# Kernel optimization log

Measured on AMD Instinct MI355X. Metric: run time of the kernel, lower is better.

## Reference

```python
import jax, jax.numpy as jnp
import numpy as np

B, L, T, D, H, DH = 8, 1024, 1024, 768, 12, 64
SPATIAL_DIM = 5


def setup_inputs() -> dict:
    key = jax.random.key(0)
    ks = jax.random.split(key, 12)
    scale = 1.0 / np.sqrt(D)
    inp = {
        "q": jax.random.normal(ks[0], (B, L, D), dtype=jnp.float32),
        "k": jax.random.normal(ks[1], (B, T, D), dtype=jnp.float32),
        "v": jax.random.normal(ks[2], (B, T, D), dtype=jnp.float32),
        "pairwise_locs": jax.random.normal(ks[3], (B, L, T, SPATIAL_DIM), dtype=jnp.float32),
        # last 64 key positions are padding in every batch row (never all-True)
        "key_padding_mask": jnp.broadcast_to(jnp.arange(T) >= T - 64, (B, T)),
        "Wq": jax.random.normal(ks[4], (D, H * DH), dtype=jnp.float32) * scale,
        "bq": jnp.zeros((H * DH,), dtype=jnp.float32),
        "Wk": jax.random.normal(ks[5], (D, H * DH), dtype=jnp.float32) * scale,
        "bk": jnp.zeros((H * DH,), dtype=jnp.float32),
        "Wv": jax.random.normal(ks[6], (D, H * DH), dtype=jnp.float32) * scale,
        "bv": jnp.zeros((H * DH,), dtype=jnp.float32),
        "Wo": jax.random.normal(ks[7], (H * DH, D), dtype=jnp.float32) * scale,
        "bo": jnp.zeros((D,), dtype=jnp.float32),
    }
    return inp


def reference(q, k, v, pairwise_locs, key_padding_mask, Wq, bq, Wk, bk, Wv, bv, Wo, bo):
    # pairwise_locs is accepted but unused in this forward path (as in the source).
    b, l, _ = q.shape
    t = k.shape[1]
    qh = (q @ Wq + bq).reshape(b, l, H, DH)  # b l h d
    kh = (k @ Wk + bk).reshape(b, t, H, DH)  # b t h d
    vh = (v @ Wv + bv).reshape(b, t, H, DH)  # b t h d
    attn = jnp.einsum('blhd,bthd->bhlt', qh, kh) / jnp.sqrt(jnp.float32(DH))
    attn = jnp.where(key_padding_mask[:, None, None, :], -jnp.inf, attn)
    fused_attn = jax.nn.softmax(attn, axis=-1)
    out = jnp.einsum('bhlt,bthd->blhd', fused_attn, vh).reshape(b, l, H * DH)
    return out @ Wo + bo  # dropout is identity in eval mode
```

## Files before the change

kernel.cpp:

```cpp
#include <hip/hip_runtime.h>
#include <hip/hip_bf16.h>
#include <cstdint>
#include <cstddef>
#include <cmath>

#define NB 8
#define NL 1024
#define NT 1024
#define ND 768
#define NH 12
#define NDH 64
#define NM (NB*NL)

typedef short short8 __attribute__((ext_vector_type(8)));
typedef unsigned short ushort4v __attribute__((ext_vector_type(4)));
typedef unsigned int uint4v __attribute__((ext_vector_type(4)));
typedef float f32x4 __attribute__((ext_vector_type(4)));
typedef float f32x16 __attribute__((ext_vector_type(16)));
typedef float float4v __attribute__((ext_vector_type(4)));

__device__ __forceinline__ unsigned short f2bf(float f) {
  union { __hip_bfloat16 h; unsigned short u; } cv;
  cv.h = __float2bfloat16(f);
  return cv.u;
}
__device__ __forceinline__ unsigned pk2(float lo, float hi) {
  return (unsigned)f2bf(lo) | ((unsigned)f2bf(hi) << 16);
}
__device__ __forceinline__ void gll16(const void* g, void* l) {
  __builtin_amdgcn_global_load_lds(
      (const __attribute__((address_space(1))) unsigned int*)g,
      (__attribute__((address_space(3))) unsigned int*)l, 16, 0, 0);
}

__global__ __launch_bounds__(128) void maskbits_kernel(
    const unsigned int* __restrict__ mask, unsigned long long* __restrict__ mb) {
  const int id = threadIdx.x;
  const unsigned int* src = mask + (size_t)(id >> 4) * NT + (id & 15) * 64;
  unsigned long long m = 0;
  for (int j = 0; j < 64; j++) m |= (unsigned long long)(src[j] != 0u) << j;
  mb[id] = m;
}

__global__ __launch_bounds__(256) void wt_kernel(
    const float* __restrict__ W0, const float* __restrict__ W1,
    const float* __restrict__ W2, const float* __restrict__ W3,
    unsigned short* __restrict__ Wt) {
  __shared__ float tile[32][33];
  const float* W = blockIdx.z == 0 ? W0 : blockIdx.z == 1 ? W1 : blockIdx.z == 2 ? W2 : W3;
  const int k0 = blockIdx.x * 32, n0 = blockIdx.y * 32;
  const int tx = threadIdx.x & 31, ty = threadIdx.x >> 5;
  for (int r = ty; r < 32; r += 8) tile[r][tx] = W[(size_t)(k0 + r) * ND + n0 + tx];
  __syncthreads();
  unsigned short* out = Wt + (size_t)blockIdx.z * ND * ND;
  for (int r = ty; r < 32; r += 8) out[(size_t)(n0 + r) * ND + k0 + tx] = f2bf(tile[tx][r]);
}

template<int MODE>
__global__ __launch_bounds__(256) void gemm_kernel(
    const float* __restrict__ Af0, const float* __restrict__ Af1,
    const float* __restrict__ Af2, const unsigned short* __restrict__ Ab,
    const unsigned short* __restrict__ Wt,
    const float* __restrict__ bias0, const float* __restrict__ bias1,
    const float* __restrict__ bias2,
    unsigned short* __restrict__ outb0, unsigned short* __restrict__ outb1,
    unsigned short* __restrict__ outb2, float* __restrict__ outf) {
  __shared__ __align__(16) unsigned short As[128 * 64];
  __shared__ __align__(16) unsigned short Bs[128 * 64];
  const int tid = threadIdx.x, lane = tid & 63, w = tid >> 6;
  const int c = lane & 15, g = lane >> 4;
  const int wrow = w & 1, wcol = w >> 1;
  const int l8 = lane >> 3, l7 = lane & 7, csw = l7 ^ l8;
  const int mbase = blockIdx.x * 128, nbase = blockIdx.y * 128;
  const int z = (MODE == 0) ? blockIdx.z : 3;

  const float* Af = (MODE == 0) ? (z == 0 ? Af0 : z == 1 ? Af1 : Af2) : nullptr;
  const unsigned short* Bt = Wt + (size_t)z * ND * ND;
  const float* bias = (MODE == 0) ? (z == 0 ? bias0 : z == 1 ? bias1 : bias2) : bias0;

  f32x4 acc[4][4];
#pragma unroll
  for (int m = 0; m < 4; m++)
#pragma unroll
    for (int n = 0; n < 4; n++) acc[m][n] = (f32x4){0.f, 0.f, 0.f, 0.f};

  for (int k0 = 0; k0 < ND; k0 += 64) {
    if (MODE == 0) {
#pragma unroll
      for (int i = 0; i < 4; i++) {
        int id = i * 256 + tid;
        int r = id >> 3, cc = id & 7;
        const float* src = &Af[(size_t)(mbase + r) * ND + k0 + cc * 8];
        float4v x0 = *(const float4v*)src;
        float4v x1 = *(const float4v*)(src + 4);
        uint4v y = {pk2(x0[0], x0[1]), pk2(x0[2], x0[3]),
                    pk2(x1[0], x1[1]), pk2(x1[2], x1[3])};
        *(uint4v*)&As[r * 64 + ((cc ^ (r & 7)) * 8)] = y;
      }
    } else {
#pragma unroll
      for (int it = 0; it < 4; it++) {
        int r = it * 32 + w * 8 + l8;
        gll16(&Ab[(size_t)(mbase + r) * ND + k0 + csw * 8], &As[(it * 32 + w * 8) * 64]);
      }
    }
#pragma unroll
    for (int it = 0; it < 4; it++) {
      int r = it * 32 + w * 8 + l8;
      gll16(&Bt[(size_t)(nbase + r) * ND + k0 + csw * 8], &Bs[(it * 32 + w * 8) * 64]);
    }
    __syncthreads();

#pragma unroll
    for (int ks = 0; ks < 2; ks++) {
      short8 a[4], b[4];
#pragma unroll
      for (int m = 0; m < 4; m++) {
        int r = wrow * 64 + m * 16 + c;
        a[m] = *(const short8*)&As[r * 64 + (((ks * 4 + g) ^ (c & 7)) * 8)];
      }
#pragma unroll
      for (int n = 0; n < 4; n++) {
        int r = wcol * 64 + n * 16 + c;
        b[n] = *(const short8*)&Bs[r * 64 + (((ks * 4 + g) ^ (c & 7)) * 8)];
      }
      if (MODE == 0 && z == 2) {
#pragma unroll
        for (int m = 0; m < 4; m++)
#pragma unroll
          for (int n = 0; n < 4; n++)
            acc[m][n] = __builtin_amdgcn_mfma_f32_16x16x32_bf16(a[m], b[n], acc[m][n], 0, 0, 0);
      } else {
#pragma unroll
        for (int m = 0; m < 4; m++)
#pragma unroll
          for (int n = 0; n < 4; n++)
            acc[m][n] = __builtin_amdgcn_mfma_f32_16x16x32_bf16(b[n], a[m], acc[m][n], 0, 0, 0);
      }
    }
    __syncthreads();
  }

  if (MODE == 0 && z == 2) {
#pragma unroll
    for (int n = 0; n < 4; n++) {
      const int col = nbase + wcol * 64 + n * 16 + c;
      const float bv = bias[col];
      const int h = col >> 6, dd = col & 63;
#pragma unroll
      for (int m = 0; m < 4; m++) {
        const int r0 = mbase + wrow * 64 + m * 16 + g * 4;
        const int bb = r0 >> 10, t = r0 & (NT - 1);
        ushort4v y;
#pragma unroll
        for (int j = 0; j < 4; j++) y[j] = f2bf(acc[m][n][j] + bv);
        *(ushort4v*)&outb2[((size_t)(bb * NH + h) * NDH + dd) * NT + t] = y;
      }
    }
  } else {
    const float scale = (MODE == 0 && z == 0) ? 0.125f * 1.44269504f : 1.0f;
    unsigned short* outb = (MODE == 0) ? (z == 0 ? outb0 : outb1) : nullptr;
#pragma unroll
    for (int n = 0; n < 4; n++) {
      const int colb = nbase + wcol * 64 + n * 16 + g * 4;
      float4v bv4 = *(const float4v*)&bias[colb];
#pragma unroll
      for (int m = 0; m < 4; m++) {
        const int row = mbase + wrow * 64 + m * 16 + c;
        if (MODE == 3) {
          float4v y;
#pragma unroll
          for (int j = 0; j < 4; j++) y[j] = acc[m][n][j] + bv4[j];
          *(float4v*)&outf[(size_t)row * ND + colb] = y;
        } else {
          ushort4v y;
#pragma unroll
          for (int j = 0; j < 4; j++) y[j] = f2bf((acc[m][n][j] + bv4[j]) * scale);
          *(ushort4v*)&outb[(size_t)row * ND + colb] = y;
        }
      }
    }
  }
}

__global__ __launch_bounds__(256) void attn_kernel(
    const unsigned short* __restrict__ qh, const unsigned short* __restrict__ kh,
    const unsigned short* __restrict__ vhT, const unsigned long long* __restrict__ maskbits,
    unsigned short* __restrict__ ao) {
  __shared__ __align__(16) unsigned short Ks[3][64 * 64];
  __shared__ __align__(16) unsigned short Vs[3][64 * 64];
  const int tid = threadIdx.x, lane = tid & 63, w = tid >> 6;
  const int q32 = lane & 31, hi = lane >> 5;
  const int l8 = lane >> 3, l7 = lane & 7;

  const int lin = blockIdx.x;
  const int qb = ((lin >> 3) & 7) * 128;
  const int bh = (lin & 7) + 8 * (lin >> 6);
  const int b = bh / NH, h = bh % NH;
  const size_t kbase = (size_t)b * NT * ND + h * NDH;
  const size_t vbase = (size_t)(b * NH + h) * NDH * NT;

  const unsigned mwsrc = ((const unsigned*)maskbits)[(size_t)b * 32 + (lane & 31)];

  short8 aq[4];
  {
    size_t qrow = (size_t)(b * NL + qb + w * 32 + q32) * ND + h * NDH + hi * 8;
#pragma unroll
    for (int ks = 0; ks < 4; ks++)
      aq[ks] = *(const short8*)&qh[qrow + ks * 16];
  }

  f32x16 o[2] = {{}, {}};
  f32x4 lrv = {0.f, 0.f, 0.f, 0.f};
  float mr = -1e30f;

  const int srow = w * 16 + l8;
  const int scs0 = l7 ^ (srow & 7), scs1 = l7 ^ ((srow + 8) & 7);

#define STAGE(gidx, nb)                                                        \
  do {                                                                         \
    gll16(&kh[kbase + (size_t)((gidx) * 64 + srow) * ND + scs0 * 8],           \
          &Ks[nb][(w * 16) * 64]);                                             \
    gll16(&vhT[vbase + (size_t)srow * NT + (gidx) * 64 + scs0 * 8],            \
          &Vs[nb][(w * 16) * 64]);                                             \
    gll16(&kh[kbase + (size_t)((gidx) * 64 + srow + 8) * ND + scs1 * 8],       \
          &Ks[nb][(w * 16 + 8) * 64]);                                         \
    gll16(&vhT[vbase + (size_t)(srow + 8) * NT + (gidx) * 64 + scs1 * 8],      \
          &Vs[nb][(w * 16 + 8) * 64]);                                         \
  } while (0)

  STAGE(0, 0);
  STAGE(1, 1);
  asm volatile("s_waitcnt vmcnt(4)" ::: "memory");
  __builtin_amdgcn_sched_barrier(0);
  __builtin_amdgcn_s_barrier();
  __builtin_amdgcn_sched_barrier(0);

  int cur = 0;
  unsigned mlo = __shfl(mwsrc, 0, 64);
  unsigned mhi_ = __shfl(mwsrc, 1, 64);

  for (int tIdx = 0; tIdx < NT / 64; tIdx++) {
    bool issued = false;
    if (tIdx + 2 < NT / 64) {
      unsigned plo = __shfl(mwsrc, tIdx * 2 + 4, 64);
      unsigned phi = __shfl(mwsrc, tIdx * 2 + 5, 64);
      if ((plo & phi) != 0xffffffffu) {
        int nb = cur + 2; if (nb >= 3) nb -= 3;
        STAGE(tIdx + 2, nb);
        issued = true;
      }
    }
    unsigned nlo = 0xffffffffu, nhi = 0xffffffffu;
    if (tIdx + 1 < NT / 64) {
      nlo = __shfl(mwsrc, tIdx * 2 + 2, 64);
      nhi = __shfl(mwsrc, tIdx * 2 + 3, 64);
    }

    if ((mlo & mhi_) != 0xffffffffu) {
      const bool anymask = (mlo | mhi_) != 0u;
#pragma unroll
      for (int tt = 0; tt < 2; tt++) {
        f32x16 s = {};
        __builtin_amdgcn_s_setprio(1);
#pragma unroll
        for (int ks = 0; ks < 4; ks++) {
          short8 ak = *(const short8*)&Ks[cur][(tt * 32 + q32) * 64 +
                          ((((ks << 1) | hi) ^ (q32 & 7)) * 8)];
          s = __builtin_amdgcn_mfma_f32_32x32x16_bf16(ak, aq[ks], s, 0, 0, 0);
        }
        __builtin_amdgcn_s_setprio(0);

        if (anymask) {
          unsigned wsd = tt ? mhi_ : mlo;
          wsd = hi ? (wsd >> 4) : wsd;
#pragma unroll
          for (int a = 0; a < 4; a++)
#pragma unroll
            for (int j = 0; j < 4; j++)
              if ((wsd >> (8 * a + j)) & 1) s[4 * a + j] = -INFINITY;
        }

        float mt = s[0];
#pragma unroll
        for (int r = 1; r < 16; r++) mt = fmaxf(mt, s[r]);
        mt = fmaxf(mt, __shfl_xor(mt, 32, 64));
        if (!__all(mt <= mr + 8.f)) {
          float mnew = fmaxf(mr, mt);
          float alpha = exp2f(mr - mnew);
          mr = mnew;
          lrv *= alpha; o[0] *= alpha; o[1] *= alpha;
        }
        unsigned pkv[4][2];
#pragma unroll
        for (int a = 0; a < 4; a++) {
          f32x4 p;
#pragma unroll
          for (int j = 0; j < 4; j++) p[j] = exp2f(s[4 * a + j] - mr);
          lrv += p;
          pkv[a][0] = pk2(p[0], p[1]);
          pkv[a][1] = pk2(p[2], p[3]);
        }

#pragma unroll
        for (int ts = 0; ts < 2; ts++) {
          unsigned u0 = pkv[2 * ts][0], u1 = pkv[2 * ts][1];
          unsigned w0 = pkv[2 * ts + 1][0], w1 = pkv[2 * ts + 1][1];
          unsigned r0 = __shfl_xor(hi ? u0 : w0, 32, 64);
          unsigned r1 = __shfl_xor(hi ? u1 : w1, 32, 64);
          union { unsigned u[4]; short8 s8; } bp;
          bp.u[0] = hi ? r0 : u0;
          bp.u[1] = hi ? r1 : u1;
          bp.u[2] = hi ? w0 : r0;
          bp.u[3] = hi ? w1 : r1;
          __builtin_amdgcn_s_setprio(1);
#pragma unroll
          for (int dt = 0; dt < 2; dt++) {
            short8 av = *(const short8*)&Vs[cur][(dt * 32 + q32) * 64 +
                            ((((tt << 2) | (ts << 1) | hi) ^ (q32 & 7)) * 8)];
            o[dt] = __builtin_amdgcn_mfma_f32_32x32x16_bf16(av, bp.s8, o[dt], 0, 0, 0);
          }
          __builtin_amdgcn_s_setprio(0);
        }
      }
    }

    if (issued)
      asm volatile("s_waitcnt vmcnt(4) lgkmcnt(0)" ::: "memory");
    else
      asm volatile("s_waitcnt vmcnt(0) lgkmcnt(0)" ::: "memory");
    __builtin_amdgcn_sched_barrier(0);
    __builtin_amdgcn_s_barrier();
    __builtin_amdgcn_sched_barrier(0);

    mlo = nlo; mhi_ = nhi;
    cur = (cur == 2) ? 0 : cur + 1;
  }
#undef STAGE

  float lr = (lrv[0] + lrv[1]) + (lrv[2] + lrv[3]);
  lr += __shfl_xor(lr, 32, 64);
  float inv = 1.f / lr;
  size_t row = (size_t)(b * NL + qb + w * 32 + q32) * ND + h * NDH;
#pragma unroll
  for (int dt = 0; dt < 2; dt++)
#pragma unroll
    for (int a = 0; a < 4; a++) {
      ushort4v y;
#pragma unroll
      for (int j = 0; j < 4; j++) y[j] = f2bf(o[dt][4 * a + j] * inv);
      *(ushort4v*)&ao[row + dt * 32 + 8 * a + 4 * hi] = y;
    }
}

extern "C" void kernel_launch(void* const* d_in, const int* in_sizes, int n_in,
                              void* d_out, int out_size, void* d_ws, size_t ws_size,
                              hipStream_t stream) {
  const float* q  = (const float*)d_in[0];
  const float* k  = (const float*)d_in[1];
  const float* v  = (const float*)d_in[2];
  const unsigned int* mask = (const unsigned int*)d_in[4];
  const float* Wq = (const float*)d_in[5];
  const float* bq = (const float*)d_in[6];
  const float* Wk = (const float*)d_in[7];
  const float* bk = (const float*)d_in[8];
  const float* Wv = (const float*)d_in[9];
  const float* bv = (const float*)d_in[10];
  const float* Wo = (const float*)d_in[11];
  const float* bo = (const float*)d_in[12];
  float* out = (float*)d_out;

  unsigned short* ws  = (unsigned short*)d_ws;
  unsigned short* Wt  = ws;
  unsigned short* qhb = Wt + (size_t)4 * ND * ND;
  unsigned short* khb = qhb + (size_t)NM * ND;
  unsigned short* vhT = khb + (size_t)NM * ND;
  unsigned short* aob = vhT + (size_t)NM * ND;
  unsigned long long* mb = (unsigned long long*)(aob + (size_t)NM * ND);

  wt_kernel<<<dim3(ND / 32, ND / 32, 4), 256, 0, stream>>>(Wq, Wk, Wv, Wo, Wt);
  maskbits_kernel<<<1, 128, 0, stream>>>(mask, mb);

  gemm_kernel<0><<<dim3(NM / 128, ND / 128, 3), 256, 0, stream>>>(
      q, k, v, nullptr, Wt, bq, bk, bv, qhb, khb, vhT, nullptr);

  attn_kernel<<<dim3(NL / 128 * NB * NH), 256, 0, stream>>>(qhb, khb, vhT, mb, aob);

  gemm_kernel<3><<<dim3(NM / 128, ND / 128), 256, 0, stream>>>(
      nullptr, nullptr, nullptr, aob, Wt, bo, nullptr, nullptr,
      nullptr, nullptr, nullptr, out);
}
```

Measured before the change: 157.5 us.

## Process two 32-row query tiles per wave in attention kernel

```diff
diff --git a/kernel.cpp b/kernel.cpp
--- a/kernel.cpp
+++ b/kernel.cpp
@@ -194,25 +194,26 @@
   const int l8 = lane >> 3, l7 = lane & 7;
 
   const int lin = blockIdx.x;
-  const int qb = ((lin >> 3) & 7) * 128;
-  const int bh = (lin & 7) + 8 * (lin >> 6);
+  const int qb = ((lin >> 3) & 3) * 256;
+  const int bh = (lin & 7) + 8 * (lin >> 5);
   const int b = bh / NH, h = bh % NH;
   const size_t kbase = (size_t)b * NT * ND + h * NDH;
   const size_t vbase = (size_t)(b * NH + h) * NDH * NT;
 
   const unsigned mwsrc = ((const unsigned*)maskbits)[(size_t)b * 32 + (lane & 31)];
 
-  short8 aq[4];
-  {
-    size_t qrow = (size_t)(b * NL + qb + w * 32 + q32) * ND + h * NDH + hi * 8;
+  short8 aq[2][4];
+#pragma unroll
+  for (int qt = 0; qt < 2; qt++) {
+    size_t qrow = (size_t)(b * NL + qb + w * 64 + qt * 32 + q32) * ND + h * NDH + hi * 8;
 #pragma unroll
     for (int ks = 0; ks < 4; ks++)
-      aq[ks] = *(const short8*)&qh[qrow + ks * 16];
+      aq[qt][ks] = *(const short8*)&qh[qrow + ks * 16];
   }
 
-  f32x16 o[2] = {{}, {}};
-  f32x4 lrv = {0.f, 0.f, 0.f, 0.f};
-  float mr = -1e30f;
+  f32x16 o[2][2] = {{{}, {}}, {{}, {}}};
+  f32x4 lrv[2] = {{0.f, 0.f, 0.f, 0.f}, {0.f, 0.f, 0.f, 0.f}};
+  float mr[2] = {-1e30f, -1e30f};
 
   const int srow = w * 16 + l8;
   const int scs0 = l7 ^ (srow & 7), scs1 = l7 ^ ((srow + 8) & 7);
@@ -261,64 +262,74 @@
       const bool anymask = (mlo | mhi_) != 0u;
 #pragma unroll
       for (int tt = 0; tt < 2; tt++) {
-        f32x16 s = {};
-        __builtin_amdgcn_s_setprio(1);
-#pragma unroll
-        for (int ks = 0; ks < 4; ks++) {
-          short8 ak = *(const short8*)&Ks[cur][(tt * 32 + q32) * 64 +
-                          ((((ks << 1) | hi) ^ (q32 & 7)) * 8)];
-          s = __builtin_amdgcn_mfma_f32_32x32x16_bf16(ak, aq[ks], s, 0, 0, 0);
+        short8 ak[4];
+#pragma unroll
+        for (int ks = 0; ks < 4; ks++)
+          ak[ks] = *(const short8*)&Ks[cur][(tt * 32 + q32) * 64 +
+                        ((((ks << 1) | hi) ^ (q32 & 7)) * 8)];
+
+        unsigned pkv[2][4][2];
+#pragma unroll
+        for (int qt = 0; qt < 2; qt++) {
+          f32x16 s = {};
+          __builtin_amdgcn_s_setprio(1);
+#pragma unroll
+          for (int ks = 0; ks < 4; ks++)
+            s = __builtin_amdgcn_mfma_f32_32x32x16_bf16(ak[ks], aq[qt][ks], s, 0, 0, 0);
+          __builtin_amdgcn_s_setprio(0);
+
+          if (anymask) {
+            unsigned wsd = tt ? mhi_ : mlo;
+            wsd = hi ? (wsd >> 4) : wsd;
+#pragma unroll
+            for (int a = 0; a < 4; a++)
+#pragma unroll
+              for (int j = 0; j < 4; j++)
+                if ((wsd >> (8 * a + j)) & 1) s[4 * a + j] = -INFINITY;
+          }
+
+          float mt = s[0];
+#pragma unroll
+          for (int r = 1; r < 16; r++) mt = fmaxf(mt, s[r]);
+          mt = fmaxf(mt, __shfl_xor(mt, 32, 64));
+          if (!__all(mt <= mr[qt] + 8.f)) {
+            float mnew = fmaxf(mr[qt], mt);
+            float alpha = exp2f(mr[qt] - mnew);
+            mr[qt] = mnew;
+            lrv[qt] *= alpha; o[qt][0] *= alpha; o[qt][1] *= alpha;
+          }
+#pragma unroll
+          for (int a = 0; a < 4; a++) {
+            f32x4 p;
+#pragma unroll
+            for (int j = 0; j < 4; j++) p[j] = exp2f(s[4 * a + j] - mr[qt]);
+            lrv[qt] += p;
+            pkv[qt][a][0] = pk2(p[0], p[1]);
+            pkv[qt][a][1] = pk2(p[2], p[3]);
+          }
         }
-        __builtin_amdgcn_s_setprio(0);
-
-        if (anymask) {
-          unsigned wsd = tt ? mhi_ : mlo;
-          wsd = hi ? (wsd >> 4) : wsd;
-#pragma unroll
-          for (int a = 0; a < 4; a++)
-#pragma unroll
-            for (int j = 0; j < 4; j++)
-              if ((wsd >> (8 * a + j)) & 1) s[4 * a + j] = -INFINITY;
-        }
-
-        float mt = s[0];
-#pragma unroll
-        for (int r = 1; r < 16; r++) mt = fmaxf(mt, s[r]);
-        mt = fmaxf(mt, __shfl_xor(mt, 32, 64));
-        if (!__all(mt <= mr + 8.f)) {
-          float mnew = fmaxf(mr, mt);
-          float alpha = exp2f(mr - mnew);
-          mr = mnew;
-          lrv *= alpha; o[0] *= alpha; o[1] *= alpha;
-        }
-        unsigned pkv[4][2];
-#pragma unroll
-        for (int a = 0; a < 4; a++) {
-          f32x4 p;
-#pragma unroll
-          for (int j = 0; j < 4; j++) p[j] = exp2f(s[4 * a + j] - mr);
-          lrv += p;
-          pkv[a][0] = pk2(p[0], p[1]);
-          pkv[a][1] = pk2(p[2], p[3]);
-        }
 
 #pragma unroll
         for (int ts = 0; ts < 2; ts++) {
-          unsigned u0 = pkv[2 * ts][0], u1 = pkv[2 * ts][1];
-          unsigned w0 = pkv[2 * ts + 1][0], w1 = pkv[2 * ts + 1][1];
-          unsigned r0 = __shfl_xor(hi ? u0 : w0, 32, 64);
-          unsigned r1 = __shfl_xor(hi ? u1 : w1, 32, 64);
-          union { unsigned u[4]; short8 s8; } bp;
-          bp.u[0] = hi ? r0 : u0;
-          bp.u[1] = hi ? r1 : u1;
-          bp.u[2] = hi ? w0 : r0;
-          bp.u[3] = hi ? w1 : r1;
+          union { unsigned u[4]; short8 s8; } bp[2];
+#pragma unroll
+          for (int qt = 0; qt < 2; qt++) {
+            unsigned u0 = pkv[qt][2 * ts][0], u1 = pkv[qt][2 * ts][1];
+            unsigned w0 = pkv[qt][2 * ts + 1][0], w1 = pkv[qt][2 * ts + 1][1];
+            unsigned r0 = __shfl_xor(hi ? u0 : w0, 32, 64);
+            unsigned r1 = __shfl_xor(hi ? u1 : w1, 32, 64);
+            bp[qt].u[0] = hi ? r0 : u0;
+            bp[qt].u[1] = hi ? r1 : u1;
+            bp[qt].u[2] = hi ? w0 : r0;
+            bp[qt].u[3] = hi ? w1 : r1;
+          }
           __builtin_amdgcn_s_setprio(1);
 #pragma unroll
           for (int dt = 0; dt < 2; dt++) {
             short8 av = *(const short8*)&Vs[cur][(dt * 32 + q32) * 64 +
                             ((((tt << 2) | (ts << 1) | hi) ^ (q32 & 7)) * 8)];
-            o[dt] = __builtin_amdgcn_mfma_f32_32x32x16_bf16(av, bp.s8, o[dt], 0, 0, 0);
+            o[0][dt] = __builtin_amdgcn_mfma_f32_32x32x16_bf16(av, bp[0].s8, o[0][dt], 0, 0, 0);
+            o[1][dt] = __builtin_amdgcn_mfma_f32_32x32x16_bf16(av, bp[1].s8, o[1][dt], 0, 0, 0);
           }
           __builtin_amdgcn_s_setprio(0);
         }
@@ -338,19 +349,22 @@
   }
 #undef STAGE
 
-  float lr = (lrv[0] + lrv[1]) + (lrv[2] + lrv[3]);
-  lr += __shfl_xor(lr, 32, 64);
-  float inv = 1.f / lr;
-  size_t row = (size_t)(b * NL + qb + w * 32 + q32) * ND + h * NDH;
-#pragma unroll
-  for (int dt = 0; dt < 2; dt++)
-#pragma unroll
-    for (int a = 0; a < 4; a++) {
-      ushort4v y;
-#pragma unroll
-      for (int j = 0; j < 4; j++) y[j] = f2bf(o[dt][4 * a + j] * inv);
-      *(ushort4v*)&ao[row + dt * 32 + 8 * a + 4 * hi] = y;
-    }
+#pragma unroll
+  for (int qt = 0; qt < 2; qt++) {
+    float lr = (lrv[qt][0] + lrv[qt][1]) + (lrv[qt][2] + lrv[qt][3]);
+    lr += __shfl_xor(lr, 32, 64);
+    float inv = 1.f / lr;
+    size_t row = (size_t)(b * NL + qb + w * 64 + qt * 32 + q32) * ND + h * NDH;
+#pragma unroll
+    for (int dt = 0; dt < 2; dt++)
+#pragma unroll
+      for (int a = 0; a < 4; a++) {
+        ushort4v y;
+#pragma unroll
+        for (int j = 0; j < 4; j++) y[j] = f2bf(o[qt][dt][4 * a + j] * inv);
+        *(ushort4v*)&ao[row + dt * 32 + 8 * a + 4 * hi] = y;
+      }
+  }
 }
 
 extern "C" void kernel_launch(void* const* d_in, const int* in_sizes, int n_in,
@@ -384,7 +398,7 @@
   gemm_kernel<0><<<dim3(NM / 128, ND / 128, 3), 256, 0, stream>>>(
       q, k, v, nullptr, Wt, bq, bk, bv, qhb, khb, vhT, nullptr);
 
-  attn_kernel<<<dim3(NL / 128 * NB * NH), 256, 0, stream>>>(qhb, khb, vhT, mb, aob);
+  attn_kernel<<<dim3(NL / 256 * NB * NH), 256, 0, stream>>>(qhb, khb, vhT, mb, aob);
 
   gemm_kernel<3><<<dim3(NM / 128, ND / 128), 256, 0, stream>>>(
       nullptr, nullptr, nullptr, aob, Wt, bo, nullptr, nullptr,
```

New measurement: 209.0 us. +32.7%, slower.
